# Optimization experiments

Measured on AMD Instinct MI355X. Metric: run time of the kernel, lower is better.

## Reference

```python
import jax, jax.numpy as jnp
import numpy as np

N, D, H, L = 100000, 128, 4, 2
C = D // H  # per-head channels
E = 1600000
NEG_SLOPE = 0.2
LN_EPS = 1e-5


def setup_inputs() -> dict:
    key = jax.random.key(0)
    ks = jax.random.split(key, 8)
    x = jax.random.normal(ks[0], (N, D), dtype=jnp.float32)
    edge_index = jax.random.randint(ks[1], (2, E), 0, N, dtype=jnp.int64)
    s = 1.0 / np.sqrt(D)
    Wl = jax.random.normal(ks[2], (L, D, D), dtype=jnp.float32) * s
    Wr = jax.random.normal(ks[3], (L, D, D), dtype=jnp.float32) * s
    att = jax.random.normal(ks[4], (L, H, C), dtype=jnp.float32) * (1.0 / np.sqrt(C))
    bias = jnp.zeros((L, D), dtype=jnp.float32)
    gamma = jnp.ones((L, D), dtype=jnp.float32)
    beta = jnp.zeros((L, D), dtype=jnp.float32)
    return {"x": x, "edge_index": edge_index, "Wl": Wl, "Wr": Wr,
            "att": att, "bias": bias, "gamma": gamma, "beta": beta}


def _gatv2_layer(h, src, dst, Wl, Wr, att, bias):
    # h: (N, D); src/dst: (E2,) with self-loops already appended
    xl = (h @ Wl).reshape(N, H, C)  # source-side transform
    xr = (h @ Wr).reshape(N, H, C)  # target-side transform
    e = jax.nn.leaky_relu(xl[src] + xr[dst], NEG_SLOPE)      # (E2, H, C)
    alpha = jnp.einsum('ehc,hc->eh', e, att)                 # (E2, H)
    # segment softmax over incoming edges of each destination node
    m = jax.ops.segment_max(alpha, dst, num_segments=N)      # (N, H)
    ea = jnp.exp(alpha - m[dst])
    s = jax.ops.segment_sum(ea, dst, num_segments=N)         # (N, H)
    a = ea / s[dst]                                          # (E2, H)
    out = jax.ops.segment_sum(a[:, :, None] * xl[src], dst, num_segments=N)
    return out.reshape(N, D) + bias


def _layer_norm(y, gamma, beta):
    mu = jnp.mean(y, axis=-1, keepdims=True)
    var = jnp.var(y, axis=-1, keepdims=True)
    return (y - mu) * jax.lax.rsqrt(var + LN_EPS) * gamma + beta


def reference(x, edge_index, Wl, Wr, att, bias, gamma, beta):
    # PyG GATv2Conv defaults: add_self_loops=True (eval mode: dropouts identity)
    loops = jnp.arange(N, dtype=edge_index.dtype)
    src = jnp.concatenate([edge_index[0], loops])
    dst = jnp.concatenate([edge_index[1], loops])
    h = x
    for l in range(L):
        g = _gatv2_layer(h, src, dst, Wl[l], Wr[l], att[l], bias[l])
        h = h + jax.nn.elu(_layer_norm(g, gamma[l], beta[l]))
    return h
```

## Files before the change

kernel.cpp:

```cpp
#include <hip/hip_runtime.h>
#include <hip/hip_fp16.h>
#include <math.h>

#define N_NODES 100000
#define D_FEAT  128
#define E_EDGES 1600000
#define E2      (E_EDGES + N_NODES)
#define NEG_SLOPE 0.2f
#define LN_EPS    1e-5f

#define NB   391
#define TS   8192
#define NTIL ((E2 + TS - 1) / TS)

typedef __attribute__((ext_vector_type(8))) short short8;
typedef __attribute__((ext_vector_type(4))) float floatx4;
typedef _Float16 h2 __attribute__((ext_vector_type(2)));

static __device__ __forceinline__ float fdot2f(h2 a, h2 b, float c) {
#if __has_builtin(__builtin_amdgcn_fdot2)
    return __builtin_amdgcn_fdot2(a, b, c, false);
#else
    return (float)a[0] * (float)b[0] + (float)a[1] * (float)b[1] + c;
#endif
}

__global__ __launch_bounds__(1024) void tile_count(const int* __restrict__ edge_dst,
                                                   int* __restrict__ tcnt) {
    __shared__ int h[NB];
    const int t = threadIdx.x;
    if (t < NB) h[t] = 0;
    __syncthreads();
    const int base = blockIdx.x * TS;
#pragma unroll
    for (int j = 0; j < TS / 1024; ++j) {
        int i = base + j * 1024 + t;
        if (i < E2) {
            int d = (i < E_EDGES) ? edge_dst[i] : (i - E_EDGES);
            atomicAdd(&h[d >> 8], 1);
        }
    }
    __syncthreads();
    if (t < NB) tcnt[blockIdx.x * NB + t] = h[t];
}

__global__ __launch_bounds__(256) void col_scan(const int* __restrict__ tcnt,
                                                int* __restrict__ toff,
                                                int* __restrict__ bcnt) {
    __shared__ int s[256];
    const int b = blockIdx.x;
    const int t = threadIdx.x;
    int v = (t < NTIL) ? tcnt[t * NB + b] : 0;
    s[t] = v;
    __syncthreads();
    for (int off = 1; off < 256; off <<= 1) {
        int x = (t >= off) ? s[t - off] : 0;
        __syncthreads();
        s[t] += x;
        __syncthreads();
    }
    if (t < NTIL) toff[t * NB + b] = s[t] - v;
    if (t == 255) bcnt[b] = s[255];
}

__global__ __launch_bounds__(512) void bucket_scan(const int* __restrict__ bcnt,
                                                   int* __restrict__ bstart,
                                                   int* __restrict__ rowstart) {
    __shared__ int s[512];
    const int t = threadIdx.x;
    int v = (t < NB) ? bcnt[t] : 0;
    s[t] = v;
    __syncthreads();
    for (int off = 1; off < 512; off <<= 1) {
        int x = (t >= off) ? s[t - off] : 0;
        __syncthreads();
        s[t] += x;
        __syncthreads();
    }
    if (t <= NB) bstart[t] = s[t] - v;
    if (t == 0) rowstart[N_NODES] = E2;
}

__global__ __launch_bounds__(1024) void tile_scatter(const int* __restrict__ edge_src,
                                                     const int* __restrict__ edge_dst,
                                                     const int* __restrict__ bstart,
                                                     const int* __restrict__ toff,
                                                     unsigned* __restrict__ pairbuf) {
    __shared__ int base[NB];
    __shared__ int cur[NB];
    const int t = threadIdx.x;
    if (t < NB) { base[t] = bstart[t] + toff[blockIdx.x * NB + t]; cur[t] = 0; }
    __syncthreads();
    const int tb = blockIdx.x * TS;
#pragma unroll
    for (int j = 0; j < TS / 1024; ++j) {
        int i = tb + j * 1024 + t;
        if (i < E2) {
            int d, sr;
            if (i < E_EDGES) { d = edge_dst[i]; sr = edge_src[i]; }
            else             { d = i - E_EDGES; sr = d; }
            int b = d >> 8;
            int rank = atomicAdd(&cur[b], 1);
            pairbuf[base[b] + rank] = (unsigned)sr | ((unsigned)(d & 255) << 17);
        }
    }
}

__global__ __launch_bounds__(1024) void bucketize(const unsigned* __restrict__ pairbuf,
                                                  const int* __restrict__ bstart,
                                                  int* __restrict__ rowstart,
                                                  int* __restrict__ csr_src) {
    __shared__ int cnt[256], sc[256], cur[256];
    const int blk = blockIdx.x;
    const int t = threadIdx.x;
    const int nbase = blk << 8;
    if (t < 256) cnt[t] = 0;
    __syncthreads();
    const int e0 = bstart[blk], e1 = bstart[blk + 1];
    for (int p = e0 + t; p < e1; p += 1024)
        atomicAdd(&cnt[pairbuf[p] >> 17], 1);
    __syncthreads();
    int v = (t < 256) ? cnt[t] : 0;
    if (t < 256) sc[t] = v;
    __syncthreads();
    for (int off = 1; off < 256; off <<= 1) {
        int x = (t < 256 && t >= off) ? sc[t - off] : 0;
        __syncthreads();
        if (t < 256) sc[t] += x;
        __syncthreads();
    }
    if (t < 256) {
        int excl = sc[t] - v;
        int node = nbase + t;
        if (node < N_NODES) rowstart[node] = e0 + excl;
        cur[t] = e0 + excl;
    }
    __syncthreads();
    for (int p = e0 + t; p < e1; p += 1024) {
        unsigned pr = pairbuf[p];
        int pos = atomicAdd(&cur[pr >> 17], 1);
        csr_src[pos] = (int)(pr & 0x1FFFF);
    }
}

static __device__ __forceinline__ unsigned short f2bf(float f) {
    unsigned u = __float_as_uint(f);
    unsigned r = (u + 0x7fffu + ((u >> 16) & 1u)) >> 16;
    return (unsigned short)r;
}

__global__ void prep_wt(const float* __restrict__ Wl, const float* __restrict__ Wr,
                        const float* __restrict__ att,
                        unsigned short* __restrict__ Wt, _Float16* __restrict__ atth) {
    int idx = blockIdx.x * 256 + threadIdx.x;
    if (idx < 65536) {
        int l    = idx >> 15;
        int rem  = idx & 32767;
        int side = rem >> 14;
        int cw   = rem & 16383;
        int col  = cw >> 7, k = cw & 127;
        const float* W = side ? Wr : Wl;
        Wt[idx] = f2bf(W[l * 16384 + k * 128 + col]);
    } else if (idx < 65536 + 256) {
        int j = idx - 65536;
        atth[j] = (_Float16)att[j];
    }
}

__global__ __launch_bounds__(256) void gemm_mfma2(
        const unsigned short* __restrict__ hbf,
        const float* __restrict__ Afp,
        const unsigned short* __restrict__ Wt,
        _Float16* __restrict__ xl, _Float16* __restrict__ xr, int n_rows) {
    const int wave = threadIdx.x >> 6;
    const int lane = threadIdx.x & 63;
    const int m = lane & 15;
    const int q = lane >> 4;
    const int r0 = (blockIdx.x * 4 + wave) * 32;

    int arow0 = r0 + m;        if (arow0 >= n_rows) arow0 = n_rows - 1;
    int arow1 = r0 + 16 + m;   if (arow1 >= n_rows) arow1 = n_rows - 1;

    floatx4 acc[2][2][8];
#pragma unroll
    for (int s = 0; s < 2; ++s)
#pragma unroll
        for (int rt = 0; rt < 2; ++rt)
#pragma unroll
            for (int ct = 0; ct < 8; ++ct) acc[s][rt][ct] = (floatx4){0.f,0.f,0.f,0.f};

#pragma unroll
    for (int ks = 0; ks < 4; ++ks) {
        const int k0 = ks * 32 + q * 8;
        short8 a0, a1;
        if (Afp) {
            float4 f0 = *(const float4*)(Afp + (size_t)arow0 * 128 + k0);
            float4 f1 = *(const float4*)(Afp + (size_t)arow0 * 128 + k0 + 4);
            float4 g0 = *(const float4*)(Afp + (size_t)arow1 * 128 + k0);
            float4 g1 = *(const float4*)(Afp + (size_t)arow1 * 128 + k0 + 4);
            a0 = (short8){(short)f2bf(f0.x), (short)f2bf(f0.y), (short)f2bf(f0.z), (short)f2bf(f0.w),
                          (short)f2bf(f1.x), (short)f2bf(f1.y), (short)f2bf(f1.z), (short)f2bf(f1.w)};
            a1 = (short8){(short)f2bf(g0.x), (short)f2bf(g0.y), (short)f2bf(g0.z), (short)f2bf(g0.w),
                          (short)f2bf(g1.x), (short)f2bf(g1.y), (short)f2bf(g1.z), (short)f2bf(g1.w)};
        } else {
            a0 = *(const short8*)(hbf + (size_t)arow0 * 128 + k0);
            a1 = *(const short8*)(hbf + (size_t)arow1 * 128 + k0);
        }
#pragma unroll
        for (int s = 0; s < 2; ++s) {
#pragma unroll
            for (int ct = 0; ct < 8; ++ct) {
                short8 b = *(const short8*)(Wt + (size_t)s * 16384
                                            + (size_t)(ct * 16 + m) * 128 + k0);
                acc[s][0][ct] = __builtin_amdgcn_mfma_f32_16x16x32_bf16(a0, b, acc[s][0][ct], 0, 0, 0);
                acc[s][1][ct] = __builtin_amdgcn_mfma_f32_16x16x32_bf16(a1, b, acc[s][1][ct], 0, 0, 0);
            }
        }
    }

#pragma unroll
    for (int s = 0; s < 2; ++s) {
        _Float16* out = s ? xr : xl;
#pragma unroll
        for (int rt = 0; rt < 2; ++rt)
#pragma unroll
            for (int ct = 0; ct < 8; ++ct)
#pragma unroll
                for (int i = 0; i < 4; ++i) {
                    int row = r0 + rt * 16 + q * 4 + i;
                    if (row < n_rows)
                        out[(size_t)row * 128 + ct * 16 + m] = (_Float16)acc[s][rt][ct][i];
                }
    }
}

union U16 { uint4 u; h2 h[4]; };

__global__ __launch_bounds__(256) void gat_node6(
        const _Float16* __restrict__ xl,
        const _Float16* __restrict__ xr,
        const float* __restrict__ h_in,
        const int* __restrict__ rowstart, const int* __restrict__ csr_src,
        const _Float16* __restrict__ atth, const float* __restrict__ bias,
        const float* __restrict__ gamma, const float* __restrict__ beta,
        float* __restrict__ h_out, unsigned* __restrict__ hbf_out) {
    __shared__ float lacc[4][8 * 136];
    __shared__ float lS[4][4];

    const int wave = threadIdx.x >> 6;
    const int lane = threadIdx.x & 63;
    const int node = blockIdx.x * 4 + wave;
    const int esub = lane >> 3;
    const int r    = lane & 7;
    const int c0   = r * 16;

    U16 xra, xrb, ata, atb;
    {
        const uint4* xp = (const uint4*)(xr + (size_t)node * 128 + c0);
        xra.u = xp[0]; xrb.u = xp[1];
        const uint4* ap = (const uint4*)(atth + c0);
        ata.u = ap[0]; atb.u = ap[1];
    }
    const h2 ns2 = {(_Float16)NEG_SLOPE, (_Float16)NEG_SLOPE};

    const int p0 = rowstart[node], p1 = rowstart[node + 1];
    float s = 0.f;
    h2 acc2[8];
#pragma unroll
    for (int j = 0; j < 8; ++j) acc2[j] = (h2){(_Float16)0.f, (_Float16)0.f};

    const unsigned short* xls = (const unsigned short*)xl;

    int pb = p0;
    bool vA = (p0 + esub) < p1;
    U16 a0, a1, b0, b1;
    {
        int pc = vA ? (p0 + esub) : (p1 - 1);
        int src = csr_src[pc];
        const uint4* rp = (const uint4*)(xls + (size_t)src * 128 + c0);
        a0.u = rp[0]; a1.u = rp[1];
    }
    bool vB = false;
    if (p0 + 8 < p1) {
        vB = (p0 + 8 + esub) < p1;
        int pc = vB ? (p0 + 8 + esub) : (p1 - 1);
        int src = csr_src[pc];
        const uint4* rp = (const uint4*)(xls + (size_t)src * 128 + c0);
        b0.u = rp[0]; b1.u = rp[1];
    }

    while (pb < p1) {
        U16 c0v, c1v;
        bool vC = false;
        if (pb + 16 < p1) {
            vC = (pb + 16 + esub) < p1;
            int pc = vC ? (pb + 16 + esub) : (p1 - 1);
            int src = csr_src[pc];
            const uint4* rp = (const uint4*)(xls + (size_t)src * 128 + c0);
            c0v.u = rp[0]; c1v.u = rp[1];
        }

        float d = 0.f;
#pragma unroll
        for (int qq = 0; qq < 4; ++qq) {
            h2 z  = a0.h[qq] + xra.h[qq];
            h2 lk = __builtin_elementwise_max(z, z * ns2);
            d = fdot2f(lk, ata.h[qq], d);
        }
#pragma unroll
        for (int qq = 0; qq < 4; ++qq) {
            h2 z  = a1.h[qq] + xrb.h[qq];
            h2 lk = __builtin_elementwise_max(z, z * ns2);
            d = fdot2f(lk, atb.h[qq], d);
        }
        float alpha = d + __shfl_xor(d, 1);
        float w = vA ? __expf(alpha) : 0.f;
        s += w;
        h2 w2 = {(_Float16)w, (_Float16)w};
#pragma unroll
        for (int qq = 0; qq < 4; ++qq)
            acc2[qq] = w2 * a0.h[qq] + acc2[qq];
#pragma unroll
        for (int qq = 0; qq < 4; ++qq)
            acc2[qq + 4] = w2 * a1.h[qq] + acc2[qq + 4];

        a0 = b0; a1 = b1; vA = vB;
        b0 = c0v; b1 = c1v; vB = vC;
        pb += 8;
    }

    float ssum = s;
    ssum += __shfl_xor(ssum, 8);
    ssum += __shfl_xor(ssum, 16);
    ssum += __shfl_xor(ssum, 32);

    float* lb = &lacc[wave][esub * 136 + c0];
#pragma unroll
    for (int qq = 0; qq < 4; ++qq) {
        h2 lo = acc2[2 * qq], hi = acc2[2 * qq + 1];
        float4 o = {(float)lo[0], (float)lo[1], (float)hi[0], (float)hi[1]};
        *(float4*)(lb + 4 * qq) = o;
    }
    if (esub == 0 && (r & 1) == 0) lS[wave][r >> 1] = ssum;

    const int c = lane * 2;
    float S = lS[wave][lane >> 4];
    float g0 = 0.f, g1 = 0.f;
#pragma unroll
    for (int e = 0; e < 8; ++e) {
        float2 f = *(const float2*)(&lacc[wave][e * 136 + c]);
        g0 += f.x; g1 += f.y;
    }
    const float invS = 1.f / S;
    g0 = g0 * invS + bias[c];
    g1 = g1 * invS + bias[c + 1];

    float sum = g0 + g1, sq = g0 * g0 + g1 * g1;
#pragma unroll
    for (int off = 1; off < 64; off <<= 1) {
        sum += __shfl_xor(sum, off);
        sq  += __shfl_xor(sq, off);
    }
    float mu   = sum * (1.f / 128.f);
    float var  = sq * (1.f / 128.f) - mu * mu;
    float rstd = rsqrtf(var + LN_EPS);
    float y0 = (g0 - mu) * rstd * gamma[c]     + beta[c];
    float y1 = (g1 - mu) * rstd * gamma[c + 1] + beta[c + 1];
    float e0 = (y0 > 0.f) ? y0 : (__expf(y0) - 1.f);
    float e1 = (y1 > 0.f) ? y1 : (__expf(y1) - 1.f);

    const float2 hv = *(const float2*)(h_in + (size_t)node * 128 + c);
    float2 o;
    o.x = hv.x + e0;
    o.y = hv.y + e1;
    *(float2*)(h_out + (size_t)node * 128 + c) = o;
    if (hbf_out) {
        unsigned pk = (unsigned)f2bf(o.x) | ((unsigned)f2bf(o.y) << 16);
        hbf_out[(size_t)node * 64 + lane] = pk;
    }
}

extern "C" void kernel_launch(void* const* d_in, const int* in_sizes, int n_in,
                              void* d_out, int out_size, void* d_ws, size_t ws_size,
                              hipStream_t stream) {
    const float* x     = (const float*)d_in[0];
    const int*   eidx  = (const int*)d_in[1];
    const float* Wl    = (const float*)d_in[2];
    const float* Wr    = (const float*)d_in[3];
    const float* att   = (const float*)d_in[4];
    const float* bias  = (const float*)d_in[5];
    const float* gamma = (const float*)d_in[6];
    const float* beta  = (const float*)d_in[7];
    float* out = (float*)d_out;

    char* ws = (char*)d_ws;
    _Float16* xl = (_Float16*)ws;              ws += (size_t)N_NODES * 128 * 2;
    _Float16* xr = (_Float16*)ws;              ws += (size_t)N_NODES * 128 * 2;
    float* h1 = (float*)ws;                    ws += (size_t)N_NODES * 128 * 4;
    unsigned short* hbf = (unsigned short*)ws; ws += (size_t)N_NODES * 128 * 2;
    unsigned short* Wt  = (unsigned short*)ws; ws += (size_t)65536 * 2;
    _Float16* atth = (_Float16*)ws;            ws += 256 * 2;
    unsigned* pairbuf = (unsigned*)ws;         ws += (size_t)E2 * 4;
    int* tcnt     = (int*)ws; ws += (size_t)NTIL * NB * 4;
    int* toff     = (int*)ws; ws += (size_t)NTIL * NB * 4;
    int* bcnt     = (int*)ws; ws += (NB + 1) * 4;
    int* bstart   = (int*)ws; ws += (NB + 1) * 4;
    int* rowstart = (int*)ws; ws += (size_t)(N_NODES + 4) * 4;
    int* csr_src  = (int*)ws; ws += (size_t)E2 * 4;

    const int* edge_src = eidx;
    const int* edge_dst = eidx + E_EDGES;

    prep_wt<<<257, 256, 0, stream>>>(Wl, Wr, att, Wt, atth);

    tile_count<<<NTIL, 1024, 0, stream>>>(edge_dst, tcnt);
    col_scan<<<NB, 256, 0, stream>>>(tcnt, toff, bcnt);
    bucket_scan<<<1, 512, 0, stream>>>(bcnt, bstart, rowstart);
    tile_scatter<<<NTIL, 1024, 0, stream>>>(edge_src, edge_dst, bstart, toff, pairbuf);
    bucketize<<<NB, 1024, 0, stream>>>(pairbuf, bstart, rowstart, csr_src);

    const int gemm_gx = (N_NODES + 127) / 128;
    for (int l = 0; l < 2; ++l) {
        const float* hin  = (l == 0) ? x  : h1;
        float*       hout = (l == 1) ? out : h1;
        gemm_mfma2<<<gemm_gx, 256, 0, stream>>>(
            hbf, (l == 0) ? x : nullptr, Wt + (size_t)l * 32768, xl, xr, N_NODES);
        gat_node6<<<N_NODES / 4, 256, 0, stream>>>(
            xl, xr, hin, rowstart, csr_src,
            atth + l * 128, bias + l * 128, gamma + l * 128, beta + l * 128,
            hout, (l == 0) ? (unsigned*)hbf : nullptr);
    }
}
```

Measured before the change: 399.0 us.

## Use ping-pong register prefetch and shuffle-based cross-edge reduction in GAT node kernel

The edge loop now alternates between two register buffers and loads the source index early, issuing the next row gather after the current edge has been consumed. This removes the three-stage register rotation copies and keeps the gather two steps ahead. The final reduction over the 8 edge sub-lanes now uses a butterfly of fp16 xor shuffles in place of the shared-memory staging buffer, so LDS use and the associated synchronization go away. Each lane ends up owning a different channel pair, and the reduction sums in fp16, which may lose a little precision compared with the previous fp32 sum.

```diff
diff --git a/kernel.cpp b/kernel.cpp
--- a/kernel.cpp
+++ b/kernel.cpp
@@ -23,6 +23,12 @@
 #else
     return (float)a[0] * (float)b[0] + (float)a[1] * (float)b[1] + c;
 #endif
+}
+
+static __device__ __forceinline__ h2 shfl_xor_h2(h2 v, int off) {
+    int i = __builtin_bit_cast(int, v);
+    i = __shfl_xor(i, off);
+    return __builtin_bit_cast(h2, i);
 }
 
 __global__ __launch_bounds__(1024) void tile_count(const int* __restrict__ edge_dst,
@@ -236,7 +242,7 @@
 
 union U16 { uint4 u; h2 h[4]; };
 
-__global__ __launch_bounds__(256) void gat_node6(
+__global__ __launch_bounds__(256) void gat_node7(
         const _Float16* __restrict__ xl,
         const _Float16* __restrict__ xr,
         const float* __restrict__ h_in,
@@ -244,9 +250,6 @@
         const _Float16* __restrict__ atth, const float* __restrict__ bias,
         const float* __restrict__ gamma, const float* __restrict__ beta,
         float* __restrict__ h_out, unsigned* __restrict__ hbf_out) {
-    __shared__ float lacc[4][8 * 136];
-    __shared__ float lS[4][4];
-
     const int wave = threadIdx.x >> 6;
     const int lane = threadIdx.x & 63;
     const int node = blockIdx.x * 4 + wave;
@@ -271,9 +274,34 @@
 
     const unsigned short* xls = (const unsigned short*)xl;
 
-    int pb = p0;
+    auto consume = [&](const U16& u0, const U16& u1, bool v) {
+        float d = 0.f;
+#pragma unroll
+        for (int qq = 0; qq < 4; ++qq) {
+            h2 z  = u0.h[qq] + xra.h[qq];
+            h2 lk = __builtin_elementwise_max(z, z * ns2);
+            d = fdot2f(lk, ata.h[qq], d);
+        }
+#pragma unroll
+        for (int qq = 0; qq < 4; ++qq) {
+            h2 z  = u1.h[qq] + xrb.h[qq];
+            h2 lk = __builtin_elementwise_max(z, z * ns2);
+            d = fdot2f(lk, atb.h[qq], d);
+        }
+        float alpha = d + __shfl_xor(d, 1);
+        float w = v ? __expf(alpha) : 0.f;
+        s += w;
+        h2 w2 = {(_Float16)w, (_Float16)w};
+#pragma unroll
+        for (int qq = 0; qq < 4; ++qq)
+            acc2[qq] = w2 * u0.h[qq] + acc2[qq];
+#pragma unroll
+        for (int qq = 0; qq < 4; ++qq)
+            acc2[qq + 4] = w2 * u1.h[qq] + acc2[qq + 4];
+    };
+
+    U16 a0, a1, b0, b1;
     bool vA = (p0 + esub) < p1;
-    U16 a0, a1, b0, b1;
     {
         int pc = vA ? (p0 + esub) : (p1 - 1);
         int src = csr_src[pc];
@@ -287,46 +315,41 @@
         int src = csr_src[pc];
         const uint4* rp = (const uint4*)(xls + (size_t)src * 128 + c0);
         b0.u = rp[0]; b1.u = rp[1];
-    }
-
-    while (pb < p1) {
-        U16 c0v, c1v;
-        bool vC = false;
-        if (pb + 16 < p1) {
-            vC = (pb + 16 + esub) < p1;
-            int pc = vC ? (pb + 16 + esub) : (p1 - 1);
-            int src = csr_src[pc];
-            const uint4* rp = (const uint4*)(xls + (size_t)src * 128 + c0);
-            c0v.u = rp[0]; c1v.u = rp[1];
-        }
-
-        float d = 0.f;
-#pragma unroll
-        for (int qq = 0; qq < 4; ++qq) {
-            h2 z  = a0.h[qq] + xra.h[qq];
-            h2 lk = __builtin_elementwise_max(z, z * ns2);
-            d = fdot2f(lk, ata.h[qq], d);
-        }
-#pragma unroll
-        for (int qq = 0; qq < 4; ++qq) {
-            h2 z  = a1.h[qq] + xrb.h[qq];
-            h2 lk = __builtin_elementwise_max(z, z * ns2);
-            d = fdot2f(lk, atb.h[qq], d);
-        }
-        float alpha = d + __shfl_xor(d, 1);
-        float w = vA ? __expf(alpha) : 0.f;
-        s += w;
-        h2 w2 = {(_Float16)w, (_Float16)w};
-#pragma unroll
-        for (int qq = 0; qq < 4; ++qq)
-            acc2[qq] = w2 * a0.h[qq] + acc2[qq];
-#pragma unroll
-        for (int qq = 0; qq < 4; ++qq)
-            acc2[qq + 4] = w2 * a1.h[qq] + acc2[qq + 4];
-
-        a0 = b0; a1 = b1; vA = vB;
-        b0 = c0v; b1 = c1v; vB = vC;
+    } else { b0 = a0; b1 = a1; }
+
+    int pb = p0;
+    while (true) {
+        bool doPf = (pb + 16) < p1;
+        int srcP = 0; bool nv = false;
+        if (doPf) {
+            nv = (pb + 16 + esub) < p1;
+            int pc = nv ? (pb + 16 + esub) : (p1 - 1);
+            srcP = csr_src[pc];
+        }
+        consume(a0, a1, vA);
+        if (doPf) {
+            const uint4* rp = (const uint4*)(xls + (size_t)srcP * 128 + c0);
+            a0.u = rp[0]; a1.u = rp[1];
+        }
+        vA = nv;
         pb += 8;
+        if (pb >= p1) break;
+
+        doPf = (pb + 16) < p1;
+        srcP = 0; nv = false;
+        if (doPf) {
+            nv = (pb + 16 + esub) < p1;
+            int pc = nv ? (pb + 16 + esub) : (p1 - 1);
+            srcP = csr_src[pc];
+        }
+        consume(b0, b1, vB);
+        if (doPf) {
+            const uint4* rp = (const uint4*)(xls + (size_t)srcP * 128 + c0);
+            b0.u = rp[0]; b1.u = rp[1];
+        }
+        vB = nv;
+        pb += 8;
+        if (pb >= p1) break;
     }
 
     float ssum = s;
@@ -334,26 +357,32 @@
     ssum += __shfl_xor(ssum, 16);
     ssum += __shfl_xor(ssum, 32);
 
-    float* lb = &lacc[wave][esub * 136 + c0];
-#pragma unroll
-    for (int qq = 0; qq < 4; ++qq) {
-        h2 lo = acc2[2 * qq], hi = acc2[2 * qq + 1];
-        float4 o = {(float)lo[0], (float)lo[1], (float)hi[0], (float)hi[1]};
-        *(float4*)(lb + 4 * qq) = o;
-    }
-    if (esub == 0 && (r & 1) == 0) lS[wave][r >> 1] = ssum;
-
-    const int c = lane * 2;
-    float S = lS[wave][lane >> 4];
-    float g0 = 0.f, g1 = 0.f;
-#pragma unroll
-    for (int e = 0; e < 8; ++e) {
-        float2 f = *(const float2*)(&lacc[wave][e * 136 + c]);
-        g0 += f.x; g1 += f.y;
-    }
-    const float invS = 1.f / S;
-    g0 = g0 * invS + bias[c];
-    g1 = g1 * invS + bias[c + 1];
+    const bool sel0 = (esub & 1) != 0;
+    const bool sel1 = ((esub >> 1) & 1) != 0;
+    const bool sel2 = ((esub >> 2) & 1) != 0;
+    h2 b4[4];
+#pragma unroll
+    for (int k = 0; k < 4; ++k) {
+        h2 keep = sel0 ? acc2[2 * k + 1] : acc2[2 * k];
+        h2 send = sel0 ? acc2[2 * k]     : acc2[2 * k + 1];
+        b4[k] = keep + shfl_xor_h2(send, 8);
+    }
+    h2 c2[2];
+#pragma unroll
+    for (int k = 0; k < 2; ++k) {
+        h2 keep = sel1 ? b4[2 * k + 1] : b4[2 * k];
+        h2 send = sel1 ? b4[2 * k]     : b4[2 * k + 1];
+        c2[k] = keep + shfl_xor_h2(send, 16);
+    }
+    h2 keepf = sel2 ? c2[1] : c2[0];
+    h2 sendf = sel2 ? c2[0] : c2[1];
+    h2 tot = keepf + shfl_xor_h2(sendf, 32);
+
+    const int c = c0 + 2 * esub;
+    const float invS = 1.f / ssum;
+    const float2 bi = *(const float2*)(bias + c);
+    float g0 = (float)tot[0] * invS + bi.x;
+    float g1 = (float)tot[1] * invS + bi.y;
 
     float sum = g0 + g1, sq = g0 * g0 + g1 * g1;
 #pragma unroll
@@ -364,8 +393,10 @@
     float mu   = sum * (1.f / 128.f);
     float var  = sq * (1.f / 128.f) - mu * mu;
     float rstd = rsqrtf(var + LN_EPS);
-    float y0 = (g0 - mu) * rstd * gamma[c]     + beta[c];
-    float y1 = (g1 - mu) * rstd * gamma[c + 1] + beta[c + 1];
+    const float2 ga = *(const float2*)(gamma + c);
+    const float2 be = *(const float2*)(beta + c);
+    float y0 = (g0 - mu) * rstd * ga.x + be.x;
+    float y1 = (g1 - mu) * rstd * ga.y + be.y;
     float e0 = (y0 > 0.f) ? y0 : (__expf(y0) - 1.f);
     float e1 = (y1 > 0.f) ? y1 : (__expf(y1) - 1.f);
 
@@ -376,7 +407,7 @@
     *(float2*)(h_out + (size_t)node * 128 + c) = o;
     if (hbf_out) {
         unsigned pk = (unsigned)f2bf(o.x) | ((unsigned)f2bf(o.y) << 16);
-        hbf_out[(size_t)node * 64 + lane] = pk;
+        hbf_out[(size_t)node * 64 + (c >> 1)] = pk;
     }
 }
 
@@ -425,7 +456,7 @@
         float*       hout = (l == 1) ? out : h1;
         gemm_mfma2<<<gemm_gx, 256, 0, stream>>>(
             hbf, (l == 0) ? x : nullptr, Wt + (size_t)l * 32768, xl, xr, N_NODES);
-        gat_node6<<<N_NODES / 4, 256, 0, stream>>>(
+        gat_node7<<<N_NODES / 4, 256, 0, stream>>>(
             xl, xr, hin, rowstart, csr_src,
             atth + l * 128, bias + l * 128, gamma + l * 128, beta + l * 128,
             hout, (l == 0) ? (unsigned*)hbf : nullptr);
```

Result: no change. 405.8 us (+1.7%).
